# Optimization experiments

Measured on AMD Instinct MI355X. Metric: run time of the kernel, lower is better.

Reference implementation:

```python
import jax, jax.numpy as jnp
import numpy as np

N_NODES = 50000
N_EDGES = 800000
NDIM_IN = 64
EDIM = 64
NDIM_OUT = 64


def setup_inputs() -> dict:
    key = jax.random.key(0)
    ks = jax.random.split(key, 8)
    nfeats = jax.random.normal(ks[0], (N_NODES, 1, NDIM_IN), dtype=jnp.float32)
    efeats = jax.random.normal(ks[1], (N_EDGES, 1, EDIM), dtype=jnp.float32)
    src = jax.random.randint(ks[2], (N_EDGES,), 0, N_NODES)
    dst = jax.random.randint(ks[3], (N_EDGES,), 0, N_NODES)
    # Linear params (PyTorch layout: [out_features, in_features]), scaled ~1/sqrt(fan_in)
    W_apply_w = jax.random.normal(ks[4], (NDIM_OUT, NDIM_IN + EDIM), dtype=jnp.float32) / np.sqrt(NDIM_IN + EDIM)
    W_apply_b = jax.random.normal(ks[5], (NDIM_OUT,), dtype=jnp.float32) * 0.01
    edge_w = jax.random.normal(ks[6], (EDIM, 2 * NDIM_OUT + EDIM), dtype=jnp.float32) / np.sqrt(2 * NDIM_OUT + EDIM)
    edge_b = jax.random.normal(ks[7], (EDIM,), dtype=jnp.float32) * 0.01
    return {"nfeats": nfeats, "efeats": efeats, "src": src, "dst": dst,
            "W_apply_w": W_apply_w, "W_apply_b": W_apply_b,
            "edge_w": edge_w, "edge_b": edge_b}


def reference(nfeats, efeats, src, dst, W_apply_w, W_apply_b, edge_w, edge_b):
    N = nfeats.shape[0]
    # --- update_all with message = edge feature, reduce = mean over incoming edges ---
    seg_sum = jax.ops.segment_sum(efeats, dst, num_segments=N)            # [N,1,edim]
    cnt = jax.ops.segment_sum(jnp.ones((efeats.shape[0],), efeats.dtype), dst, num_segments=N)
    h_neigh = seg_sum / jnp.maximum(cnt, 1.0)[:, None, None]              # DGL mean -> 0 for isolated nodes
    # --- apply: relu(W_apply([h || h_neigh])) ---
    cat = jnp.concatenate([nfeats, h_neigh], axis=2)                      # [N,1,ndim_in+edim]
    h = jax.nn.relu(jnp.einsum('nid,od->nio', cat, W_apply_w) + W_apply_b)  # [N,1,ndim_out]
    # --- edge update: relu(edge_layer([h_src || h_dst || e])) ---
    ecat = jnp.concatenate([h[src], h[dst], efeats], axis=-1)             # [E,1,2*ndim_out+edim]
    eh = jax.nn.relu(jnp.einsum('eid,od->eio', ecat, edge_w) + edge_b)    # [E,1,edim]
    return (h, eh)
```

## Files before the change

kernel.cpp:

```cpp
#include <hip/hip_runtime.h>
#include <hip/hip_bf16.h>

#define N_NODES 50000
#define N_EDGES 800000
#define NSCANB 49

typedef __attribute__((ext_vector_type(8))) __bf16 bf16x8;
typedef __attribute__((ext_vector_type(4))) float f32x4;

static __device__ __forceinline__ bf16x8 cvt8(float4 a, float4 b) {
    bf16x8 r;
    r[0] = (__bf16)a.x; r[1] = (__bf16)a.y; r[2] = (__bf16)a.z; r[3] = (__bf16)a.w;
    r[4] = (__bf16)b.x; r[5] = (__bf16)b.y; r[6] = (__bf16)b.z; r[7] = (__bf16)b.w;
    return r;
}

__global__ void hist_kernel(const int* __restrict__ dst, int* __restrict__ deg) {
    int e = blockIdx.x * 256 + threadIdx.x;
    atomicAdd(&deg[dst[e]], 1);
}

__global__ __launch_bounds__(1024) void scanA_kernel(const int* __restrict__ deg,
                                                     int* __restrict__ starts,
                                                     int* __restrict__ btot) {
    __shared__ int buf[1024];
    int t = threadIdx.x;
    int i = blockIdx.x * 1024 + t;
    int v = (i < N_NODES) ? deg[i] : 0;
    int val = v;
    buf[t] = v;
    __syncthreads();
    for (int off = 1; off < 1024; off <<= 1) {
        int add = (t >= off) ? buf[t - off] : 0;
        __syncthreads();
        val += add;
        buf[t] = val;
        __syncthreads();
    }
    if (i < N_NODES) starts[i] = val - v;
    if (t == 1023) btot[blockIdx.x] = val;
}

__global__ void scanB_kernel(int* __restrict__ btot, int* __restrict__ starts) {
    if (threadIdx.x == 0 && blockIdx.x == 0) {
        int run = 0;
        for (int b = 0; b < NSCANB; ++b) { int v = btot[b]; btot[b] = run; run += v; }
        starts[N_NODES] = run;
    }
}

__global__ __launch_bounds__(1024) void scanC_kernel(int* __restrict__ starts,
                                                     int* __restrict__ cursor,
                                                     const int* __restrict__ btot) {
    int i = blockIdx.x * 1024 + threadIdx.x;
    if (i < N_NODES) {
        int s = starts[i] + btot[blockIdx.x];
        starts[i] = s;
        cursor[i] = s;
    }
}

__global__ void bucket_kernel(const int* __restrict__ dst, int* __restrict__ cursor,
                              int* __restrict__ csr) {
    int e = blockIdx.x * 256 + threadIdx.x;
    int p = atomicAdd(&cursor[dst[e]], 1);
    csr[p] = e;
}

__global__ __launch_bounds__(256) void gather_kernel(const float* __restrict__ ef,
                                                     const int* __restrict__ starts,
                                                     const int* __restrict__ csr,
                                                     float* __restrict__ h_neigh) {
    int w = threadIdx.x >> 6, lane = threadIdx.x & 63;
    int n = blockIdx.x * 4 + w;
    if (n >= N_NODES) return;
    int s = starts[n], e_end = starts[n + 1];
    float s0 = 0.f, s1 = 0.f;
    int i = s;
    for (; i + 2 <= e_end; i += 2) {
        int e0 = csr[i], e1 = csr[i + 1];
        s0 += ef[(size_t)e0 * 64 + lane];
        s1 += ef[(size_t)e1 * 64 + lane];
    }
    if (i < e_end) s0 += ef[(size_t)csr[i] * 64 + lane];
    float cnt = (float)(e_end - s);
    h_neigh[(size_t)n * 64 + lane] = (s0 + s1) / fmaxf(cnt, 1.0f);
}

__global__ void __launch_bounds__(64) node_kernel(const float* __restrict__ nfeats,
                                                  const float* __restrict__ W,
                                                  const float* __restrict__ bias,
                                                  const float* __restrict__ h_neigh,
                                                  float* __restrict__ h) {
    int n = blockIdx.x * 64 + threadIdx.x;
    if (n >= N_NODES) return;

    float acc[64];
#pragma unroll
    for (int j = 0; j < 64; ++j) acc[j] = bias[j];

    const float* __restrict__ xn = nfeats + (size_t)n * 64;
    const float* __restrict__ xs = h_neigh + (size_t)n * 64;

#pragma unroll 1
    for (int kc = 0; kc < 8; ++kc) {
        float xv[8];
#pragma unroll
        for (int i = 0; i < 8; ++i) xv[i] = xn[kc * 8 + i];
#pragma unroll
        for (int j = 0; j < 64; ++j)
#pragma unroll
            for (int i = 0; i < 8; ++i)
                acc[j] = fmaf(W[j * 128 + kc * 8 + i], xv[i], acc[j]);
    }
#pragma unroll 1
    for (int kc = 0; kc < 8; ++kc) {
        float xv[8];
#pragma unroll
        for (int i = 0; i < 8; ++i) xv[i] = xs[kc * 8 + i];
#pragma unroll
        for (int j = 0; j < 64; ++j)
#pragma unroll
            for (int i = 0; i < 8; ++i)
                acc[j] = fmaf(W[j * 128 + 64 + kc * 8 + i], xv[i], acc[j]);
    }

    float* out = h + (size_t)n * 64;
#pragma unroll
    for (int j = 0; j < 64; j += 4) {
        float4 v = make_float4(fmaxf(acc[j + 0], 0.0f), fmaxf(acc[j + 1], 0.0f),
                               fmaxf(acc[j + 2], 0.0f), fmaxf(acc[j + 3], 0.0f));
        *(float4*)(out + j) = v;
    }
}

__global__ __launch_bounds__(256) void edge_mfma_kernel(
    const float* __restrict__ efeats, const int* __restrict__ src_,
    const int* __restrict__ dst_, const float* __restrict__ h,
    const float* __restrict__ We,
    const float* __restrict__ be, float* __restrict__ eh) {
    __shared__ __bf16 Wl[64][200];
    __shared__ __bf16 efl[256][72];
    const int t = threadIdx.x;
    const int ebase = blockIdx.x * 256;

    for (int i = t; i < 1536; i += 256) {
        int r = i / 24, c = (i % 24) * 8;
        const float* wp = We + r * 192 + c;
        float4 w0 = *(const float4*)wp;
        float4 w1 = *(const float4*)(wp + 4);
        *(bf16x8*)&Wl[r][c] = cvt8(w0, w1);
    }
    for (int i = t; i < 2048; i += 256) {
        int r = i >> 3, c = (i & 7) * 8;
        const float* p = efeats + (size_t)(ebase + r) * 64 + c;
        float4 a = *(const float4*)p;
        float4 b = *(const float4*)(p + 4);
        *(bf16x8*)&efl[r][c] = cvt8(a, b);
    }
    __syncthreads();

    const int wid = t >> 6, lane = t & 63;
    const int r16 = lane & 15;
    const int g = lane >> 4;

    float4 bv[4];
#pragma unroll
    for (int m = 0; m < 4; ++m) bv[m] = *(const float4*)(be + m * 16 + g * 4);

#pragma unroll 1
    for (int grp = 0; grp < 4; ++grp) {
        const int erow = wid * 64 + grp * 16 + r16;
        const int e = ebase + erow;
        const int s = src_[e], d = dst_[e];
        const float* ps = h + (size_t)s * 64;
        const float* pd = h + (size_t)d * 64;

        bf16x8 bfr[6];
        {
            float4 a0 = *(const float4*)(ps + g * 8);
            float4 a1 = *(const float4*)(ps + g * 8 + 4);
            float4 a2 = *(const float4*)(ps + 32 + g * 8);
            float4 a3 = *(const float4*)(ps + 32 + g * 8 + 4);
            bfr[0] = cvt8(a0, a1);
            bfr[1] = cvt8(a2, a3);
            float4 b0 = *(const float4*)(pd + g * 8);
            float4 b1 = *(const float4*)(pd + g * 8 + 4);
            float4 b2 = *(const float4*)(pd + 32 + g * 8);
            float4 b3 = *(const float4*)(pd + 32 + g * 8 + 4);
            bfr[2] = cvt8(b0, b1);
            bfr[3] = cvt8(b2, b3);
            bfr[4] = *(const bf16x8*)&efl[erow][g * 8];
            bfr[5] = *(const bf16x8*)&efl[erow][32 + g * 8];
        }

        f32x4 acc[4] = {{0,0,0,0},{0,0,0,0},{0,0,0,0},{0,0,0,0}};
#pragma unroll
        for (int c = 0; c < 6; ++c) {
#pragma unroll
            for (int m = 0; m < 4; ++m) {
                bf16x8 a = *(const bf16x8*)&Wl[m * 16 + r16][c * 32 + g * 8];
                acc[m] = __builtin_amdgcn_mfma_f32_16x16x32_bf16(a, bfr[c], acc[m], 0, 0, 0);
            }
        }

        float* op = eh + (size_t)e * 64 + g * 4;
#pragma unroll
        for (int m = 0; m < 4; ++m) {
            float4 o = make_float4(fmaxf(acc[m][0] + bv[m].x, 0.0f),
                                   fmaxf(acc[m][1] + bv[m].y, 0.0f),
                                   fmaxf(acc[m][2] + bv[m].z, 0.0f),
                                   fmaxf(acc[m][3] + bv[m].w, 0.0f));
            *(float4*)(op + m * 16) = o;
        }
    }
}

extern "C" void kernel_launch(void* const* d_in, const int* in_sizes, int n_in,
                              void* d_out, int out_size, void* d_ws, size_t ws_size,
                              hipStream_t stream) {
    const float* nfeats = (const float*)d_in[0];
    const float* efeats = (const float*)d_in[1];
    const int*   src    = (const int*)d_in[2];
    const int*   dst    = (const int*)d_in[3];
    const float* Wa     = (const float*)d_in[4];
    const float* ba     = (const float*)d_in[5];
    const float* We     = (const float*)d_in[6];
    const float* be     = (const float*)d_in[7];

    float* out = (float*)d_out;
    float* h   = out;
    float* eh  = out + (size_t)N_NODES * 64;

    int*   scratch = (int*)(eh + 30000000);
    int*   deg     = scratch;
    int*   starts  = scratch + 262144;
    int*   cursor  = scratch + 524288;
    int*   btot    = scratch + 786432;
    int*   csr     = scratch + 1048576;
    float* h_neigh = (float*)(scratch + 4194304);

    hipMemsetAsync(deg, 0, N_NODES * sizeof(int), stream);

    hist_kernel <<<N_EDGES / 256, 256, 0, stream>>>(dst, deg);
    scanA_kernel<<<NSCANB, 1024, 0, stream>>>(deg, starts, btot);
    scanB_kernel<<<1, 64, 0, stream>>>(btot, starts);
    scanC_kernel<<<NSCANB, 1024, 0, stream>>>(starts, cursor, btot);
    bucket_kernel<<<N_EDGES / 256, 256, 0, stream>>>(dst, cursor, csr);
    gather_kernel<<<(N_NODES + 3) / 4, 256, 0, stream>>>(efeats, starts, csr, h_neigh);
    node_kernel <<<(N_NODES + 63) / 64, 64, 0, stream>>>(nfeats, Wa, ba, h_neigh, h);
    edge_mfma_kernel<<<N_EDGES / 256, 256, 0, stream>>>(efeats, src, dst, h, We, be, eh);
}
```

Baseline: 779.7 us.

## Use bf16 MFMA for node linear layer and single-block scan

Replaces the per-thread scalar FMA node kernel, where each thread held 64 accumulators and read weights from global memory, with an MFMA kernel. It stages the apply weights in LDS as bf16 and computes 16-node tiles per wave. It also merges the three-kernel prefix scan into one 1024-thread block, where each thread scans a 49-element chunk, removing two launches. Inputs are cast to bf16 for the node matmul, which lowers precision, and the single-block scan reads serially within each thread.

Result: faster. 721.9 us (-7.4%).

```diff
diff --git a/kernel.cpp b/kernel.cpp
--- a/kernel.cpp
+++ b/kernel.cpp
@@ -3,7 +3,7 @@
 
 #define N_NODES 50000
 #define N_EDGES 800000
-#define NSCANB 49
+#define SCHUNK 49
 
 typedef __attribute__((ext_vector_type(8))) __bf16 bf16x8;
 typedef __attribute__((ext_vector_type(4))) float f32x4;
@@ -20,16 +20,17 @@
     atomicAdd(&deg[dst[e]], 1);
 }
 
-__global__ __launch_bounds__(1024) void scanA_kernel(const int* __restrict__ deg,
-                                                     int* __restrict__ starts,
-                                                     int* __restrict__ btot) {
+__global__ __launch_bounds__(1024) void scan_kernel(const int* __restrict__ deg,
+                                                    int* __restrict__ starts,
+                                                    int* __restrict__ cursor) {
     __shared__ int buf[1024];
     int t = threadIdx.x;
-    int i = blockIdx.x * 1024 + t;
-    int v = (i < N_NODES) ? deg[i] : 0;
-    int val = v;
-    buf[t] = v;
+    int lo = t * SCHUNK, hi = min(lo + SCHUNK, N_NODES);
+    int sum = 0;
+    for (int i = lo; i < hi; ++i) sum += deg[i];
+    buf[t] = sum;
     __syncthreads();
+    int val = sum;
     for (int off = 1; off < 1024; off <<= 1) {
         int add = (t >= off) ? buf[t - off] : 0;
         __syncthreads();
@@ -37,27 +38,11 @@
         buf[t] = val;
         __syncthreads();
     }
-    if (i < N_NODES) starts[i] = val - v;
-    if (t == 1023) btot[blockIdx.x] = val;
-}
-
-__global__ void scanB_kernel(int* __restrict__ btot, int* __restrict__ starts) {
-    if (threadIdx.x == 0 && blockIdx.x == 0) {
-        int run = 0;
-        for (int b = 0; b < NSCANB; ++b) { int v = btot[b]; btot[b] = run; run += v; }
-        starts[N_NODES] = run;
-    }
-}
-
-__global__ __launch_bounds__(1024) void scanC_kernel(int* __restrict__ starts,
-                                                     int* __restrict__ cursor,
-                                                     const int* __restrict__ btot) {
-    int i = blockIdx.x * 1024 + threadIdx.x;
-    if (i < N_NODES) {
-        int s = starts[i] + btot[blockIdx.x];
-        starts[i] = s;
-        cursor[i] = s;
-    }
+    int run = val - sum;
+    for (int i = lo; i < hi; ++i) {
+        starts[i] = run; cursor[i] = run; run += deg[i];
+    }
+    if (t == 1023) starts[N_NODES] = run;
 }
 
 __global__ void bucket_kernel(const int* __restrict__ dst, int* __restrict__ cursor,
@@ -87,50 +72,75 @@
     h_neigh[(size_t)n * 64 + lane] = (s0 + s1) / fmaxf(cnt, 1.0f);
 }
 
-__global__ void __launch_bounds__(64) node_kernel(const float* __restrict__ nfeats,
-                                                  const float* __restrict__ W,
-                                                  const float* __restrict__ bias,
-                                                  const float* __restrict__ h_neigh,
-                                                  float* __restrict__ h) {
-    int n = blockIdx.x * 64 + threadIdx.x;
-    if (n >= N_NODES) return;
-
-    float acc[64];
-#pragma unroll
-    for (int j = 0; j < 64; ++j) acc[j] = bias[j];
-
-    const float* __restrict__ xn = nfeats + (size_t)n * 64;
-    const float* __restrict__ xs = h_neigh + (size_t)n * 64;
+__global__ __launch_bounds__(256) void node_mfma_kernel(
+    const float* __restrict__ nfeats, const float* __restrict__ hn,
+    const float* __restrict__ Wa,
+    const float* __restrict__ ba, float* __restrict__ h) {
+    __shared__ __bf16 Wl[64][136];
+    const int t = threadIdx.x;
+    const int nbase = blockIdx.x * 256;
+
+    for (int i = t; i < 1024; i += 256) {
+        int r = i >> 4, c = (i & 15) * 8;
+        const float* wp = Wa + r * 128 + c;
+        float4 w0 = *(const float4*)wp;
+        float4 w1 = *(const float4*)(wp + 4);
+        *(bf16x8*)&Wl[r][c] = cvt8(w0, w1);
+    }
+    __syncthreads();
+
+    const int wid = t >> 6, lane = t & 63;
+    const int r16 = lane & 15;
+    const int g = lane >> 4;
+
+    float4 bv[4];
+#pragma unroll
+    for (int m = 0; m < 4; ++m) bv[m] = *(const float4*)(ba + m * 16 + g * 4);
 
 #pragma unroll 1
-    for (int kc = 0; kc < 8; ++kc) {
-        float xv[8];
-#pragma unroll
-        for (int i = 0; i < 8; ++i) xv[i] = xn[kc * 8 + i];
-#pragma unroll
-        for (int j = 0; j < 64; ++j)
-#pragma unroll
-            for (int i = 0; i < 8; ++i)
-                acc[j] = fmaf(W[j * 128 + kc * 8 + i], xv[i], acc[j]);
-    }
-#pragma unroll 1
-    for (int kc = 0; kc < 8; ++kc) {
-        float xv[8];
-#pragma unroll
-        for (int i = 0; i < 8; ++i) xv[i] = xs[kc * 8 + i];
-#pragma unroll
-        for (int j = 0; j < 64; ++j)
-#pragma unroll
-            for (int i = 0; i < 8; ++i)
-                acc[j] = fmaf(W[j * 128 + 64 + kc * 8 + i], xv[i], acc[j]);
-    }
-
-    float* out = h + (size_t)n * 64;
-#pragma unroll
-    for (int j = 0; j < 64; j += 4) {
-        float4 v = make_float4(fmaxf(acc[j + 0], 0.0f), fmaxf(acc[j + 1], 0.0f),
-                               fmaxf(acc[j + 2], 0.0f), fmaxf(acc[j + 3], 0.0f));
-        *(float4*)(out + j) = v;
+    for (int grp = 0; grp < 4; ++grp) {
+        const int n = nbase + wid * 64 + grp * 16 + r16;
+        const int nc = (n < N_NODES) ? n : (N_NODES - 1);
+        const float* p0 = nfeats + (size_t)nc * 64;
+        const float* p1 = hn + (size_t)nc * 64;
+
+        bf16x8 bfr[4];
+        {
+            float4 a0 = *(const float4*)(p0 + g * 8);
+            float4 a1 = *(const float4*)(p0 + g * 8 + 4);
+            float4 a2 = *(const float4*)(p0 + 32 + g * 8);
+            float4 a3 = *(const float4*)(p0 + 32 + g * 8 + 4);
+            bfr[0] = cvt8(a0, a1);
+            bfr[1] = cvt8(a2, a3);
+            float4 b0 = *(const float4*)(p1 + g * 8);
+            float4 b1 = *(const float4*)(p1 + g * 8 + 4);
+            float4 b2 = *(const float4*)(p1 + 32 + g * 8);
+            float4 b3 = *(const float4*)(p1 + 32 + g * 8 + 4);
+            bfr[2] = cvt8(b0, b1);
+            bfr[3] = cvt8(b2, b3);
+        }
+
+        f32x4 acc[4] = {{0,0,0,0},{0,0,0,0},{0,0,0,0},{0,0,0,0}};
+#pragma unroll
+        for (int c = 0; c < 4; ++c) {
+#pragma unroll
+            for (int m = 0; m < 4; ++m) {
+                bf16x8 a = *(const bf16x8*)&Wl[m * 16 + r16][c * 32 + g * 8];
+                acc[m] = __builtin_amdgcn_mfma_f32_16x16x32_bf16(a, bfr[c], acc[m], 0, 0, 0);
+            }
+        }
+
+        if (n < N_NODES) {
+            float* op = h + (size_t)n * 64 + g * 4;
+#pragma unroll
+            for (int m = 0; m < 4; ++m) {
+                float4 o = make_float4(fmaxf(acc[m][0] + bv[m].x, 0.0f),
+                                       fmaxf(acc[m][1] + bv[m].y, 0.0f),
+                                       fmaxf(acc[m][2] + bv[m].z, 0.0f),
+                                       fmaxf(acc[m][3] + bv[m].w, 0.0f));
+                *(float4*)(op + m * 16) = o;
+            }
+        }
     }
 }
 
@@ -236,18 +246,15 @@
     int*   deg     = scratch;
     int*   starts  = scratch + 262144;
     int*   cursor  = scratch + 524288;
-    int*   btot    = scratch + 786432;
     int*   csr     = scratch + 1048576;
     float* h_neigh = (float*)(scratch + 4194304);
 
     hipMemsetAsync(deg, 0, N_NODES * sizeof(int), stream);
 
-    hist_kernel <<<N_EDGES / 256, 256, 0, stream>>>(dst, deg);
-    scanA_kernel<<<NSCANB, 1024, 0, stream>>>(deg, starts, btot);
-    scanB_kernel<<<1, 64, 0, stream>>>(btot, starts);
-    scanC_kernel<<<NSCANB, 1024, 0, stream>>>(starts, cursor, btot);
+    hist_kernel  <<<N_EDGES / 256, 256, 0, stream>>>(dst, deg);
+    scan_kernel  <<<1, 1024, 0, stream>>>(deg, starts, cursor);
     bucket_kernel<<<N_EDGES / 256, 256, 0, stream>>>(dst, cursor, csr);
     gather_kernel<<<(N_NODES + 3) / 4, 256, 0, stream>>>(efeats, starts, csr, h_neigh);
-    node_kernel <<<(N_NODES + 63) / 64, 64, 0, stream>>>(nfeats, Wa, ba, h_neigh, h);
+    node_mfma_kernel<<<(N_NODES + 255) / 256, 256, 0, stream>>>(nfeats, h_neigh, Wa, ba, h);
     edge_mfma_kernel<<<N_EDGES / 256, 256, 0, stream>>>(efeats, src, dst, h, We, be, eh);
 }
```
